# Performance work log

Hardware: AMD Instinct MI355X
Metric: run time of the kernel (lower is better)

Reference implementation:

```python
import jax, jax.numpy as jnp
import numpy as np

N = 50000      # nodes
E = 1600000    # edges (before self loops)
B = 512        # graphs
D = 128        # gcn dim (constant across the 3 GAT layers)
H = 1024       # hidden_dim
O = 128        # output_dim
NEG_SLOPE = 0.2


def setup_inputs() -> dict:
    key = jax.random.key(0)
    ks = jax.random.split(key, 24)
    inp = {
        "x": jax.random.normal(ks[0], (N, D), jnp.float32),
        "edge_index": jax.random.randint(ks[1], (2, E), 0, N, dtype=jnp.int64),
        "edge_weight": jax.random.uniform(ks[2], (E,), jnp.float32),
        "batch": jnp.sort(jax.random.randint(ks[3], (N,), 0, B, dtype=jnp.int64)),
    }
    s = 1.0 / np.sqrt(D)
    for i in range(3):
        k = 4 + 4 * i
        inp[f"W{i+1}"] = jax.random.normal(ks[k], (D, D), jnp.float32) * s
        inp[f"as{i+1}"] = jax.random.normal(ks[k + 1], (D,), jnp.float32) * s
        inp[f"ad{i+1}"] = jax.random.normal(ks[k + 2], (D,), jnp.float32) * s
        inp[f"b{i+1}"] = jnp.zeros((D,), jnp.float32)
    inp["Wf1"] = jax.random.normal(ks[16], (D, H), jnp.float32) * s
    inp["bf1"] = jnp.zeros((H,), jnp.float32)
    inp["Wf2"] = jax.random.normal(ks[17], (H, O), jnp.float32) * (1.0 / np.sqrt(H))
    inp["bf2"] = jnp.zeros((O,), jnp.float32)
    return inp


def gat_conv(x, src, dst, W, a_src, a_dst, b):
    """PyG GATConv, heads=1: gather -> leakyrelu -> segment softmax -> scatter-add."""
    h = x @ W                                   # [N, D]
    e = jax.nn.leaky_relu(jnp.take(h @ a_src, src) + jnp.take(h @ a_dst, dst), NEG_SLOPE)  # [E']
    m = jax.ops.segment_max(e, dst, num_segments=N)
    ex = jnp.exp(e - m[dst])
    denom = jax.ops.segment_sum(ex, dst, num_segments=N)
    alpha = ex / denom[dst]                      # segment softmax over incoming edges
    out = jax.ops.segment_sum(alpha[:, None] * h[src], dst, num_segments=N)
    return out + b


def reference(x, edge_index, edge_weight, batch,
              W1, as1, ad1, b1, W2, as2, ad2, b2, W3, as3, ad3, b3,
              Wf1, bf1, Wf2, bf2):
    # GATConv adds self loops; edge_weight is unused by GATConv (faithful to original)
    loop = jnp.arange(N, dtype=edge_index.dtype)
    src = jnp.concatenate([edge_index[0], loop])
    dst = jnp.concatenate([edge_index[1], loop])

    h = gat_conv(x, src, dst, W1, as1, ad1, b1)
    h = jax.nn.relu(gat_conv(h, src, dst, W2, as2, ad2, b2))
    h = jax.nn.relu(gat_conv(h, src, dst, W3, as3, ad3, b3))

    # global mean pool (gep)
    sums = jax.ops.segment_sum(h, batch, num_segments=B)        # [B, D]
    counts = jax.ops.segment_sum(jnp.ones((N,), h.dtype), batch, num_segments=B)
    pooled = sums / jnp.maximum(counts, 1.0)[:, None]

    # MLP head; dropout is identity at inference
    o = jax.nn.relu(pooled) @ Wf1 + bf1
    o = jax.nn.relu(o) @ Wf2 + bf2
    return o
```

## Files before the change

### kernel.cpp

```cpp
#include <hip/hip_runtime.h>
#include <cstdint>
#include <cstddef>

#define NEG_SLOPE 0.2f

typedef _Float16 f16x8 __attribute__((ext_vector_type(8)));
typedef float f32x4v __attribute__((ext_vector_type(4)));

__device__ __forceinline__ unsigned enc_f(float f) {
  unsigned u = __float_as_uint(f);
  return (u & 0x80000000u) ? ~u : (u | 0x80000000u);
}
__device__ __forceinline__ float dec_f(unsigned u) {
  return (u & 0x80000000u) ? __uint_as_float(u ^ 0x80000000u) : __uint_as_float(~u);
}

#define AST 136
#define WST 136
#define HST 132
#define SMEM_BYTES (64 * AST * 2 + 128 * WST * 2)

__global__ void k_bounds(const int* __restrict__ batch, int N, int B,
                         int* __restrict__ gstart, unsigned* __restrict__ maxPart,
                         int* __restrict__ counts) {
  int n = blockIdx.x * blockDim.x + threadIdx.x;
  if (n < 768) maxPart[n] = 0u;
  if (n >= N) return;
  counts[n] = 0;
  int cur = batch[n];
  if (n == 0) {
    for (int g = 0; g <= cur; g++) gstart[g] = 0;
  } else {
    int prev = batch[n - 1];
    for (int g = prev + 1; g <= cur; g++) gstart[g] = n;
  }
  if (n == N - 1) {
    for (int g = cur + 1; g <= B; g++) gstart[g] = N;
  }
}

__global__ void k_count_rank(const int* __restrict__ dst, int E,
                             int* counts, int* __restrict__ rank) {
  int e = blockIdx.x * blockDim.x + threadIdx.x;
  if (e < E) rank[e] = atomicAdd(&counts[dst[e]], 1);
}

__global__ __launch_bounds__(1024) void k_scan1(const int* __restrict__ counts, int N,
                                                int* __restrict__ row_ptr, int* __restrict__ part) {
  __shared__ int tmp[1024];
  int t = threadIdx.x;
  int i = blockIdx.x * 1024 + t;
  int v = (i < N) ? 1 + counts[i] : 0;
  tmp[t] = v;
  __syncthreads();
  for (int off = 1; off < 1024; off <<= 1) {
    int u = (t >= off) ? tmp[t - off] : 0;
    __syncthreads();
    tmp[t] += u;
    __syncthreads();
  }
  if (i < N) row_ptr[i + 1] = tmp[t];
  if (t == 1023) part[blockIdx.x] = tmp[t];
}

__global__ __launch_bounds__(1024) void k_scan3(int* __restrict__ row_ptr,
                                                const int* __restrict__ part, int N) {
  __shared__ int s_off;
  int bi = blockIdx.x;
  if (threadIdx.x == 0) {
    int run = 0;
    for (int b = 0; b < bi; b++) run += part[b];
    s_off = run;
    if (bi == 0) row_ptr[0] = 0;
  }
  __syncthreads();
  int i = bi * 1024 + threadIdx.x;
  if (i < N) row_ptr[i + 1] += s_off;
}

__device__ __forceinline__ void gemm_body(char* smem, float* redmax, int bx,
                                          const float* __restrict__ A32,
                                          const unsigned short* __restrict__ A16,
                                          const float* __restrict__ W,
                                          unsigned short* __restrict__ hb,
                                          const float* __restrict__ asrc,
                                          const float* __restrict__ adst,
                                          float* __restrict__ sv, float* __restrict__ dv,
                                          unsigned* __restrict__ maxSlot, int M) {
  _Float16* Ah = (_Float16*)smem;
  _Float16* Wt = (_Float16*)(smem + 64 * AST * 2);
  float*    hS = (float*)(smem + 64 * AST * 2);
  int t = threadIdx.x;
  int rowbase = bx * 64;

  if (A16) {
    for (int i = t; i < 64 * 16; i += 256) {
      int r = i >> 4, c8 = (i & 15) << 3;
      int gr = rowbase + r;
      uint4 v = make_uint4(0u, 0u, 0u, 0u);
      if (gr < M) v = *(const uint4*)&A16[(size_t)gr * 128 + c8];
      *(uint4*)&Ah[r * AST + c8] = v;
    }
  } else {
    for (int i = t; i < 64 * 32; i += 256) {
      int r = i >> 5, c4 = (i & 31) << 2;
      int gr = rowbase + r;
      float4 v = make_float4(0.f, 0.f, 0.f, 0.f);
      if (gr < M) v = *(const float4*)&A32[(size_t)gr * 128 + c4];
      _Float16 tmp[4] = {(_Float16)v.x, (_Float16)v.y, (_Float16)v.z, (_Float16)v.w};
      *(short4*)&Ah[r * AST + c4] = *(short4*)tmp;
    }
  }
  for (int i = t; i < 128 * 32; i += 256) {
    int r = i >> 5, c4 = (i & 31) << 2;
    float4 v = *(const float4*)&W[(size_t)r * 128 + c4];
    Wt[(c4 + 0) * WST + r] = (_Float16)v.x;
    Wt[(c4 + 1) * WST + r] = (_Float16)v.y;
    Wt[(c4 + 2) * WST + r] = (_Float16)v.z;
    Wt[(c4 + 3) * WST + r] = (_Float16)v.w;
  }
  __syncthreads();

  int wave = t >> 6, lane = t & 63, quad = lane >> 4, l15 = lane & 15;
  f32x4v acc[4][2];
#pragma unroll
  for (int mt = 0; mt < 4; mt++)
#pragma unroll
    for (int nt = 0; nt < 2; nt++) {
      acc[mt][nt][0] = 0.f; acc[mt][nt][1] = 0.f; acc[mt][nt][2] = 0.f; acc[mt][nt][3] = 0.f;
    }

#pragma unroll
  for (int s = 0; s < 4; s++) {
    int k0 = (s << 5) + (quad << 3);
    f16x8 af[4], bf[2];
#pragma unroll
    for (int mt = 0; mt < 4; mt++)
      af[mt] = *(f16x8*)&Ah[(mt * 16 + l15) * AST + k0];
#pragma unroll
    for (int nt = 0; nt < 2; nt++)
      bf[nt] = *(f16x8*)&Wt[(wave * 32 + nt * 16 + l15) * WST + k0];
#pragma unroll
    for (int mt = 0; mt < 4; mt++)
#pragma unroll
      for (int nt = 0; nt < 2; nt++)
        acc[mt][nt] = __builtin_amdgcn_mfma_f32_16x16x32_f16(af[mt], bf[nt], acc[mt][nt], 0, 0, 0);
  }
  __syncthreads();

#pragma unroll
  for (int mt = 0; mt < 4; mt++)
#pragma unroll
    for (int nt = 0; nt < 2; nt++)
#pragma unroll
      for (int rr = 0; rr < 4; rr++)
        hS[(mt * 16 + quad * 4 + rr) * HST + wave * 32 + nt * 16 + l15] = acc[mt][nt][rr];
  __syncthreads();

  int tx = t & 31, ty = t >> 5;
  float4 av  = *(const float4*)&asrc[tx * 4];
  float4 adv = *(const float4*)&adst[tx * 4];
  float wmax = -1e30f;
#pragma unroll
  for (int r8 = 0; r8 < 8; r8++) {
    int row = r8 * 8 + ty;
    int gr = rowbase + row;
    float4 hv = *(float4*)&hS[row * HST + tx * 4];
    float ps = hv.x * av.x + hv.y * av.y + hv.z * av.z + hv.w * av.w;
    float pd = hv.x * adv.x + hv.y * adv.y + hv.z * adv.z + hv.w * adv.w;
#pragma unroll
    for (int mask = 16; mask; mask >>= 1) {
      ps += __shfl_xor(ps, mask);
      pd += __shfl_xor(pd, mask);
    }
    if (gr < M) {
      _Float16 hq[4] = {(_Float16)hv.x, (_Float16)hv.y, (_Float16)hv.z, (_Float16)hv.w};
      *(uint2*)&hb[(size_t)gr * 128 + tx * 4] = *(uint2*)hq;
      if (tx == 0) { sv[gr] = ps; dv[gr] = pd; wmax = fmaxf(wmax, ps); }
    }
  }
#pragma unroll
  for (int mask = 32; mask; mask >>= 1) wmax = fmaxf(wmax, __shfl_xor(wmax, mask));
  if ((t & 63) == 0) redmax[t >> 6] = wmax;
  __syncthreads();
  if (t == 0) {
    float mx = fmaxf(fmaxf(redmax[0], redmax[1]), fmaxf(redmax[2], redmax[3]));
    atomicMax(&maxSlot[bx & 255], enc_f(mx));
  }
}

__global__ __launch_bounds__(256) void k_fill_gemm(const int* __restrict__ src,
                                                   const int* __restrict__ dst,
                                                   const int* __restrict__ rank, int E, int N,
                                                   const int* __restrict__ row_ptr,
                                                   int* __restrict__ col,
                                                   const float* __restrict__ A32,
                                                   const float* __restrict__ W,
                                                   unsigned short* __restrict__ hb,
                                                   const float* __restrict__ asrc,
                                                   const float* __restrict__ adst,
                                                   float* __restrict__ sv, float* __restrict__ dv,
                                                   unsigned* __restrict__ maxSlot, int Gg) {
  __shared__ __align__(16) char smem[SMEM_BYTES];
  __shared__ float redmax[4];
  int b = (int)blockIdx.x;
  bool isGemm = ((b % 9) == 4) && ((b / 9) < Gg);
  if (isGemm) {
    gemm_body(smem, redmax, b / 9, A32, (const unsigned short*)nullptr, W,
              hb, asrc, adst, sv, dv, maxSlot, N);
  } else {
    int nGemmBefore = (b >= 4) ? min((b - 4) / 9 + 1, Gg) : 0;
    int i = (b - nGemmBefore) * 256 + threadIdx.x;
    if (i < N) col[row_ptr[i]] = i;
    int e = i - N;
    if (e >= 0 && e < E) col[row_ptr[dst[e]] + 1 + rank[e]] = src[e];
  }
}

__global__ __launch_bounds__(256) void k_gemm_fused(const unsigned short* __restrict__ A16,
                                                    const float* __restrict__ W,
                                                    unsigned short* __restrict__ hb,
                                                    const float* __restrict__ asrc,
                                                    const float* __restrict__ adst,
                                                    float* __restrict__ sv, float* __restrict__ dv,
                                                    unsigned* __restrict__ maxSlot, int M) {
  __shared__ __align__(16) char smem[SMEM_BYTES];
  __shared__ float redmax[4];
  gemm_body(smem, redmax, (int)blockIdx.x, (const float*)nullptr, A16, W,
            hb, asrc, adst, sv, dv, maxSlot, M);
}

__global__ __launch_bounds__(256) void k_agg(const unsigned short* __restrict__ hb,
                                             const float* __restrict__ sv,
                                             const float* __restrict__ dv,
                                             const int* __restrict__ row_ptr,
                                             const int* __restrict__ col,
                                             const float* __restrict__ bias,
                                             const unsigned* __restrict__ maxSlot,
                                             unsigned short* __restrict__ out16,
                                             int N, int relu) {
  int wid = (int)((blockIdx.x * (size_t)blockDim.x + threadIdx.x) >> 6);
  int lane = threadIdx.x & 63;
  if (wid >= N) return;

  unsigned mp = max(max(maxSlot[lane], maxSlot[lane + 64]),
                    max(maxSlot[lane + 128], maxSlot[lane + 192]));
#pragma unroll
  for (int off = 32; off; off >>= 1) mp = max(mp, __shfl_xor(mp, off));
  float maxS = dec_f(mp);

  int beg = row_ptr[wid], end = row_ptr[wid + 1];
  float dn = dv[wid];
  float m = maxS + dn;
  m = (m > 0.f) ? m : NEG_SLOPE * m;

  int g = lane >> 4, sub = lane & 15;
  const uint32_t* hbu = (const uint32_t*)hb;
  float acc[8];
#pragma unroll
  for (int k = 0; k < 8; k++) acc[k] = 0.f;
  float dsum = 0.f;

  int j = beg + g;
  float w0 = 0.f, w1 = 0.f, w2 = 0.f;
  uint4 h0 = make_uint4(0u, 0u, 0u, 0u);
  uint4 h1 = make_uint4(0u, 0u, 0u, 0u);
  uint4 h2 = make_uint4(0u, 0u, 0u, 0u);
  if (j < end) {
    int sn = col[j];
    float e = sv[sn] + dn;
    e = (e > 0.f) ? e : NEG_SLOPE * e;
    w0 = __expf(e - m);
    h0 = *(const uint4*)(hbu + (size_t)sn * 64 + sub * 4);
  }
  if (j + 4 < end) {
    int sn = col[j + 4];
    float e = sv[sn] + dn;
    e = (e > 0.f) ? e : NEG_SLOPE * e;
    w1 = __expf(e - m);
    h1 = *(const uint4*)(hbu + (size_t)sn * 64 + sub * 4);
  }
  if (j + 8 < end) {
    int sn = col[j + 8];
    float e = sv[sn] + dn;
    e = (e > 0.f) ? e : NEG_SLOPE * e;
    w2 = __expf(e - m);
    h2 = *(const uint4*)(hbu + (size_t)sn * 64 + sub * 4);
  }
  j += 12;
  while (j < end) {
    dsum += w0;
    {
      const _Float16* hp = (const _Float16*)&h0;
#pragma unroll
      for (int k = 0; k < 8; k++) acc[k] += w0 * (float)hp[k];
    }
    w0 = w1; h0 = h1;
    w1 = w2; h1 = h2;
    int sn = col[j];
    float e = sv[sn] + dn;
    e = (e > 0.f) ? e : NEG_SLOPE * e;
    w2 = __expf(e - m);
    h2 = *(const uint4*)(hbu + (size_t)sn * 64 + sub * 4);
    j += 4;
  }
  {
    dsum += w0;
    const _Float16* hp = (const _Float16*)&h0;
#pragma unroll
    for (int k = 0; k < 8; k++) acc[k] += w0 * (float)hp[k];
  }
  {
    dsum += w1;
    const _Float16* hp = (const _Float16*)&h1;
#pragma unroll
    for (int k = 0; k < 8; k++) acc[k] += w1 * (float)hp[k];
  }
  {
    dsum += w2;
    const _Float16* hp = (const _Float16*)&h2;
#pragma unroll
    for (int k = 0; k < 8; k++) acc[k] += w2 * (float)hp[k];
  }

  dsum += __shfl_xor(dsum, 16);
  dsum += __shfl_xor(dsum, 32);
#pragma unroll
  for (int k = 0; k < 8; k++) {
    acc[k] += __shfl_xor(acc[k], 16);
    acc[k] += __shfl_xor(acc[k], 32);
  }
  if (lane < 16) {
    float inv = 1.f / dsum;
    float o[8];
    const float* bp = &bias[sub * 8];
#pragma unroll
    for (int k = 0; k < 8; k++) {
      o[k] = acc[k] * inv + bp[k];
      if (relu) o[k] = fmaxf(o[k], 0.f);
    }
    _Float16 q[8];
#pragma unroll
    for (int k = 0; k < 8; k++) q[k] = (_Float16)o[k];
    *(uint4*)&out16[(size_t)wid * 128 + sub * 8] = *(uint4*)q;
  }
}

__global__ __launch_bounds__(256) void k_pool(const unsigned short* __restrict__ h16,
                                              const int* __restrict__ gstart,
                                              float* __restrict__ pooled, int B) {
  __shared__ float red[4][128];
  int b = blockIdx.x, t = threadIdx.x;
  int c = t & 63, seg = t >> 6;
  int s0 = gstart[b], s1 = gstart[b + 1];
  int cnt = s1 - s0;
  int per = (cnt + 3) >> 2;
  int n0 = s0 + seg * per;
  int n1 = min(n0 + per, s1);
  const uint32_t* hu = (const uint32_t*)h16;
  float a0 = 0.f, a1 = 0.f;
  for (int n = n0; n < n1; n++) {
    union { uint32_t u; _Float16 h[2]; } cv;
    cv.u = hu[(size_t)n * 64 + c];
    a0 += (float)cv.h[0];
    a1 += (float)cv.h[1];
  }
  if (seg) { red[seg][2 * c] = a0; red[seg][2 * c + 1] = a1; }
  __syncthreads();
  if (seg == 0) {
    a0 += red[1][2 * c] + red[2][2 * c] + red[3][2 * c];
    a1 += red[1][2 * c + 1] + red[2][2 * c + 1] + red[3][2 * c + 1];
    float inv = 1.f / (float)(cnt > 0 ? cnt : 1);
    pooled[b * 128 + 2 * c]     = fmaxf(a0 * inv, 0.f);
    pooled[b * 128 + 2 * c + 1] = fmaxf(a1 * inv, 0.f);
  }
}

__global__ __launch_bounds__(256) void k_mlp(const float* __restrict__ pooled,
                                             const float* __restrict__ Wf1,
                                             const float* __restrict__ bf1,
                                             const float* __restrict__ Wf2,
                                             const float* __restrict__ bf2,
                                             float* __restrict__ out, int B) {
  __shared__ float P[4][128];
  __shared__ float H1[4][1024];
  __shared__ float R[4][128];
  int t = threadIdx.x;
  int g0 = blockIdx.x * 4;

  for (int i = t; i < 4 * 128; i += 256) {
    int gi = i >> 7, c = i & 127;
    P[gi][c] = (g0 + gi < B) ? pooled[(size_t)(g0 + gi) * 128 + c] : 0.f;
  }
  __syncthreads();

#pragma unroll
  for (int cb = 0; cb < 4; cb++) {
    int c = cb * 256 + t;
    float a0 = 0.f, a1 = 0.f, a2 = 0.f, a3 = 0.f;
    for (int k = 0; k < 128; k++) {
      float w = Wf1[(size_t)k * 1024 + c];
      a0 += P[0][k] * w; a1 += P[1][k] * w; a2 += P[2][k] * w; a3 += P[3][k] * w;
    }
    float b = bf1[c];
    H1[0][c] = fmaxf(a0 + b, 0.f);
    H1[1][c] = fmaxf(a1 + b, 0.f);
    H1[2][c] = fmaxf(a2 + b, 0.f);
    H1[3][c] = fmaxf(a3 + b, 0.f);
  }
  __syncthreads();

  int c = t & 127, hh = t >> 7;
  float a0 = 0.f, a1 = 0.f, a2 = 0.f, a3 = 0.f;
  int k0 = hh * 512;
  for (int k = k0; k < k0 + 512; k++) {
    float w = Wf2[(size_t)k * 128 + c];
    a0 += H1[0][k] * w; a1 += H1[1][k] * w; a2 += H1[2][k] * w; a3 += H1[3][k] * w;
  }
  if (hh == 1) { R[0][c] = a0; R[1][c] = a1; R[2][c] = a2; R[3][c] = a3; }
  __syncthreads();
  if (hh == 0) {
    float b = bf2[c];
    float o0 = a0 + R[0][c] + b;
    float o1 = a1 + R[1][c] + b;
    float o2 = a2 + R[2][c] + b;
    float o3 = a3 + R[3][c] + b;
    if (g0 + 0 < B) out[(size_t)(g0 + 0) * 128 + c] = o0;
    if (g0 + 1 < B) out[(size_t)(g0 + 1) * 128 + c] = o1;
    if (g0 + 2 < B) out[(size_t)(g0 + 2) * 128 + c] = o2;
    if (g0 + 3 < B) out[(size_t)(g0 + 3) * 128 + c] = o3;
  }
}

extern "C" void kernel_launch(void* const* d_in, const int* in_sizes, int n_in,
                              void* d_out, int out_size, void* d_ws, size_t ws_size,
                              hipStream_t stream) {
  const float* x     = (const float*)d_in[0];
  const int*   ei    = (const int*)d_in[1];
  const int*   batch = (const int*)d_in[3];
  const float* W1 = (const float*)d_in[4];
  const float* as1 = (const float*)d_in[5];
  const float* ad1 = (const float*)d_in[6];
  const float* b1 = (const float*)d_in[7];
  const float* W2 = (const float*)d_in[8];
  const float* as2 = (const float*)d_in[9];
  const float* ad2 = (const float*)d_in[10];
  const float* b2 = (const float*)d_in[11];
  const float* W3 = (const float*)d_in[12];
  const float* as3 = (const float*)d_in[13];
  const float* ad3 = (const float*)d_in[14];
  const float* b3 = (const float*)d_in[15];
  const float* Wf1 = (const float*)d_in[16];
  const float* bf1 = (const float*)d_in[17];
  const float* Wf2 = (const float*)d_in[18];
  const float* bf2 = (const float*)d_in[19];

  const int N = in_sizes[0] / 128;
  const int E = in_sizes[1] / 2;
  const int B = out_size / 128;

  char* base_ws = (char*)d_ws;
  size_t off = 0;
  auto carve = [&](size_t bytes) -> void* {
    off = (off + 255) & ~(size_t)255;
    void* p = base_ws + off;
    off += bytes;
    return p;
  };
  int* counts   = (int*)carve((size_t)N * 4);
  int* row_ptr  = (int*)carve((size_t)(N + 1) * 4);
  int* rank     = (int*)carve((size_t)E * 4);
  int* col      = (int*)carve((size_t)(E + N) * 4);
  int* part     = (int*)carve(1024 * 4);
  int* gstart   = (int*)carve((size_t)(B + 1) * 4);
  unsigned* maxPart = (unsigned*)carve(768 * 4);
  float* sbuf   = (float*)carve((size_t)N * 4);
  float* dbuf   = (float*)carve((size_t)N * 4);
  unsigned short* hb  = (unsigned short*)carve((size_t)N * 128 * 2);
  unsigned short* a16 = (unsigned short*)carve((size_t)N * 128 * 2);
  float* pooled = (float*)carve((size_t)B * 128 * 4);

  const int* srcp = ei;
  const int* dstp = ei + E;
  const int nb = (N + 1023) / 1024;
  const int Gg = (N + 63) / 64;
  const int Gf = (E + N + 255) / 256;

  hipLaunchKernelGGL(k_bounds, dim3((N + 255) / 256), dim3(256), 0, stream,
                     batch, N, B, gstart, maxPart, counts);
  hipLaunchKernelGGL(k_count_rank, dim3((E + 255) / 256), dim3(256), 0, stream,
                     dstp, E, counts, rank);
  hipLaunchKernelGGL(k_scan1, dim3(nb), dim3(1024), 0, stream, counts, N, row_ptr, part);
  hipLaunchKernelGGL(k_scan3, dim3(nb), dim3(1024), 0, stream, row_ptr, part, N);

  hipLaunchKernelGGL(k_fill_gemm, dim3(Gf + Gg), dim3(256), 0, stream,
                     srcp, dstp, rank, E, N, row_ptr, col,
                     x, W1, hb, as1, ad1, sbuf, dbuf, maxPart + 0 * 256, Gg);

  hipLaunchKernelGGL(k_agg, dim3((N + 3) / 4), dim3(256), 0, stream,
                     hb, sbuf, dbuf, row_ptr, col, b1, maxPart + 0 * 256, a16, N, 0);

  hipLaunchKernelGGL(k_gemm_fused, dim3(Gg), dim3(256), 0, stream,
                     a16, W2, hb, as2, ad2, sbuf, dbuf, maxPart + 1 * 256, N);
  hipLaunchKernelGGL(k_agg, dim3((N + 3) / 4), dim3(256), 0, stream,
                     hb, sbuf, dbuf, row_ptr, col, b2, maxPart + 1 * 256, a16, N, 1);

  hipLaunchKernelGGL(k_gemm_fused, dim3(Gg), dim3(256), 0, stream,
                     a16, W3, hb, as3, ad3, sbuf, dbuf, maxPart + 2 * 256, N);
  hipLaunchKernelGGL(k_agg, dim3((N + 3) / 4), dim3(256), 0, stream,
                     hb, sbuf, dbuf, row_ptr, col, b3, maxPart + 2 * 256, a16, N, 1);

  hipLaunchKernelGGL(k_pool, dim3(B), dim3(256), 0, stream, a16, gstart, pooled, B);
  hipLaunchKernelGGL(k_mlp, dim3((B + 3) / 4), dim3(256), 0, stream,
                     pooled, Wf1, bf1, Wf2, bf2, (float*)d_out, B);
}
```

Baseline: 527.9 us.

## Fuse preprocessing and pooling kernels to cut launch count

Zeroing of counts and maxPart moves to a single memset, and the edge count/rank pass is merged with the graph-bounds pass into one launch. The two-pass scan becomes a single kernel that recomputes each block's prefix offset by summing all earlier counts. Global mean pooling is folded into the MLP head kernel, which drops the pooled buffer. This removes several launches and intermediate round trips, but the scan now reads earlier counts redundantly in every block and the pool stage runs on only 128 blocks instead of 512.

```diff
diff --git a/kernel.cpp b/kernel.cpp
--- a/kernel.cpp
+++ b/kernel.cpp
@@ -20,36 +20,46 @@
 #define HST 132
 #define SMEM_BYTES (64 * AST * 2 + 128 * WST * 2)
 
-__global__ void k_bounds(const int* __restrict__ batch, int N, int B,
-                         int* __restrict__ gstart, unsigned* __restrict__ maxPart,
-                         int* __restrict__ counts) {
-  int n = blockIdx.x * blockDim.x + threadIdx.x;
-  if (n < 768) maxPart[n] = 0u;
-  if (n >= N) return;
-  counts[n] = 0;
-  int cur = batch[n];
-  if (n == 0) {
-    for (int g = 0; g <= cur; g++) gstart[g] = 0;
+__global__ void k_count_bounds(const int* __restrict__ dst, int E,
+                               int* counts, int* __restrict__ rank, int Ec,
+                               const int* __restrict__ batch, int N, int B,
+                               int* __restrict__ gstart) {
+  if ((int)blockIdx.x < Ec) {
+    int e = blockIdx.x * 256 + threadIdx.x;
+    if (e < E) rank[e] = atomicAdd(&counts[dst[e]], 1);
   } else {
-    int prev = batch[n - 1];
-    for (int g = prev + 1; g <= cur; g++) gstart[g] = n;
-  }
-  if (n == N - 1) {
-    for (int g = cur + 1; g <= B; g++) gstart[g] = N;
-  }
-}
-
-__global__ void k_count_rank(const int* __restrict__ dst, int E,
-                             int* counts, int* __restrict__ rank) {
-  int e = blockIdx.x * blockDim.x + threadIdx.x;
-  if (e < E) rank[e] = atomicAdd(&counts[dst[e]], 1);
-}
-
-__global__ __launch_bounds__(1024) void k_scan1(const int* __restrict__ counts, int N,
-                                                int* __restrict__ row_ptr, int* __restrict__ part) {
+    int n = (blockIdx.x - Ec) * 256 + threadIdx.x;
+    if (n >= N) return;
+    int cur = batch[n];
+    if (n == 0) {
+      for (int g = 0; g <= cur; g++) gstart[g] = 0;
+    } else {
+      int prev = batch[n - 1];
+      for (int g = prev + 1; g <= cur; g++) gstart[g] = n;
+    }
+    if (n == N - 1) {
+      for (int g = cur + 1; g <= B; g++) gstart[g] = N;
+    }
+  }
+}
+
+__global__ __launch_bounds__(1024) void k_scan_all(const int* __restrict__ counts, int N,
+                                                   int* __restrict__ row_ptr) {
   __shared__ int tmp[1024];
-  int t = threadIdx.x;
-  int i = blockIdx.x * 1024 + t;
+  __shared__ int s_off;
+  int bi = blockIdx.x, t = threadIdx.x;
+  int hi = bi * 1024;
+  int base = 0;
+  for (int i = t; i < hi; i += 1024) base += counts[i];
+  tmp[t] = base;
+  __syncthreads();
+  for (int off = 512; off; off >>= 1) {
+    if (t < off) tmp[t] += tmp[t + off];
+    __syncthreads();
+  }
+  if (t == 0) s_off = tmp[0] + hi;
+  __syncthreads();
+  int i = hi + t;
   int v = (i < N) ? 1 + counts[i] : 0;
   tmp[t] = v;
   __syncthreads();
@@ -59,23 +69,8 @@
     tmp[t] += u;
     __syncthreads();
   }
-  if (i < N) row_ptr[i + 1] = tmp[t];
-  if (t == 1023) part[blockIdx.x] = tmp[t];
-}
-
-__global__ __launch_bounds__(1024) void k_scan3(int* __restrict__ row_ptr,
-                                                const int* __restrict__ part, int N) {
-  __shared__ int s_off;
-  int bi = blockIdx.x;
-  if (threadIdx.x == 0) {
-    int run = 0;
-    for (int b = 0; b < bi; b++) run += part[b];
-    s_off = run;
-    if (bi == 0) row_ptr[0] = 0;
-  }
-  __syncthreads();
-  int i = bi * 1024 + threadIdx.x;
-  if (i < N) row_ptr[i + 1] += s_off;
+  if (i < N) row_ptr[i + 1] = tmp[t] + s_off;
+  if (bi == 0 && t == 0) row_ptr[0] = 0;
 }
 
 __device__ __forceinline__ void gemm_body(char* smem, float* redmax, int bx,
@@ -346,89 +341,85 @@
   }
 }
 
-__global__ __launch_bounds__(256) void k_pool(const unsigned short* __restrict__ h16,
-                                              const int* __restrict__ gstart,
-                                              float* __restrict__ pooled, int B) {
-  __shared__ float red[4][128];
-  int b = blockIdx.x, t = threadIdx.x;
-  int c = t & 63, seg = t >> 6;
-  int s0 = gstart[b], s1 = gstart[b + 1];
-  int cnt = s1 - s0;
-  int per = (cnt + 3) >> 2;
-  int n0 = s0 + seg * per;
-  int n1 = min(n0 + per, s1);
-  const uint32_t* hu = (const uint32_t*)h16;
-  float a0 = 0.f, a1 = 0.f;
-  for (int n = n0; n < n1; n++) {
-    union { uint32_t u; _Float16 h[2]; } cv;
-    cv.u = hu[(size_t)n * 64 + c];
-    a0 += (float)cv.h[0];
-    a1 += (float)cv.h[1];
-  }
-  if (seg) { red[seg][2 * c] = a0; red[seg][2 * c + 1] = a1; }
-  __syncthreads();
-  if (seg == 0) {
-    a0 += red[1][2 * c] + red[2][2 * c] + red[3][2 * c];
-    a1 += red[1][2 * c + 1] + red[2][2 * c + 1] + red[3][2 * c + 1];
-    float inv = 1.f / (float)(cnt > 0 ? cnt : 1);
-    pooled[b * 128 + 2 * c]     = fmaxf(a0 * inv, 0.f);
-    pooled[b * 128 + 2 * c + 1] = fmaxf(a1 * inv, 0.f);
-  }
-}
-
-__global__ __launch_bounds__(256) void k_mlp(const float* __restrict__ pooled,
-                                             const float* __restrict__ Wf1,
-                                             const float* __restrict__ bf1,
-                                             const float* __restrict__ Wf2,
-                                             const float* __restrict__ bf2,
-                                             float* __restrict__ out, int B) {
+__global__ __launch_bounds__(256) void k_poolmlp(const unsigned short* __restrict__ h16,
+                                                 const int* __restrict__ gstart,
+                                                 const float* __restrict__ Wf1,
+                                                 const float* __restrict__ bf1,
+                                                 const float* __restrict__ Wf2,
+                                                 const float* __restrict__ bf2,
+                                                 float* __restrict__ out, int B) {
   __shared__ float P[4][128];
   __shared__ float H1[4][1024];
   __shared__ float R[4][128];
+  __shared__ float red[4][128];
   int t = threadIdx.x;
   int g0 = blockIdx.x * 4;
-
-  for (int i = t; i < 4 * 128; i += 256) {
-    int gi = i >> 7, c = i & 127;
-    P[gi][c] = (g0 + gi < B) ? pooled[(size_t)(g0 + gi) * 128 + c] : 0.f;
-  }
-  __syncthreads();
+  int c = t & 63, seg = t >> 6;
+  const uint32_t* hu = (const uint32_t*)h16;
+
+  for (int gi = 0; gi < 4; gi++) {
+    int g = g0 + gi;
+    int s0 = 0, s1 = 0;
+    if (g < B) { s0 = gstart[g]; s1 = gstart[g + 1]; }
+    int cnt = s1 - s0;
+    int per = (cnt + 3) >> 2;
+    int n0 = s0 + seg * per;
+    int n1 = min(n0 + per, s1);
+    float a0 = 0.f, a1 = 0.f;
+    for (int n = n0; n < n1; n++) {
+      union { uint32_t u; _Float16 h[2]; } cv;
+      cv.u = hu[(size_t)n * 64 + c];
+      a0 += (float)cv.h[0];
+      a1 += (float)cv.h[1];
+    }
+    red[seg][2 * c] = a0;
+    red[seg][2 * c + 1] = a1;
+    __syncthreads();
+    if (seg == 0) {
+      float b0 = red[0][2 * c] + red[1][2 * c] + red[2][2 * c] + red[3][2 * c];
+      float b1 = red[0][2 * c + 1] + red[1][2 * c + 1] + red[2][2 * c + 1] + red[3][2 * c + 1];
+      float inv = 1.f / (float)(cnt > 0 ? cnt : 1);
+      P[gi][2 * c]     = fmaxf(b0 * inv, 0.f);
+      P[gi][2 * c + 1] = fmaxf(b1 * inv, 0.f);
+    }
+    __syncthreads();
+  }
 
 #pragma unroll
   for (int cb = 0; cb < 4; cb++) {
-    int c = cb * 256 + t;
+    int cc = cb * 256 + t;
     float a0 = 0.f, a1 = 0.f, a2 = 0.f, a3 = 0.f;
     for (int k = 0; k < 128; k++) {
-      float w = Wf1[(size_t)k * 1024 + c];
+      float w = Wf1[(size_t)k * 1024 + cc];
       a0 += P[0][k] * w; a1 += P[1][k] * w; a2 += P[2][k] * w; a3 += P[3][k] * w;
     }
-    float b = bf1[c];
-    H1[0][c] = fmaxf(a0 + b, 0.f);
-    H1[1][c] = fmaxf(a1 + b, 0.f);
-    H1[2][c] = fmaxf(a2 + b, 0.f);
-    H1[3][c] = fmaxf(a3 + b, 0.f);
-  }
-  __syncthreads();
-
-  int c = t & 127, hh = t >> 7;
+    float b = bf1[cc];
+    H1[0][cc] = fmaxf(a0 + b, 0.f);
+    H1[1][cc] = fmaxf(a1 + b, 0.f);
+    H1[2][cc] = fmaxf(a2 + b, 0.f);
+    H1[3][cc] = fmaxf(a3 + b, 0.f);
+  }
+  __syncthreads();
+
+  int cc = t & 127, hh = t >> 7;
   float a0 = 0.f, a1 = 0.f, a2 = 0.f, a3 = 0.f;
   int k0 = hh * 512;
   for (int k = k0; k < k0 + 512; k++) {
-    float w = Wf2[(size_t)k * 128 + c];
+    float w = Wf2[(size_t)k * 128 + cc];
     a0 += H1[0][k] * w; a1 += H1[1][k] * w; a2 += H1[2][k] * w; a3 += H1[3][k] * w;
   }
-  if (hh == 1) { R[0][c] = a0; R[1][c] = a1; R[2][c] = a2; R[3][c] = a3; }
+  if (hh == 1) { R[0][cc] = a0; R[1][cc] = a1; R[2][cc] = a2; R[3][cc] = a3; }
   __syncthreads();
   if (hh == 0) {
-    float b = bf2[c];
-    float o0 = a0 + R[0][c] + b;
-    float o1 = a1 + R[1][c] + b;
-    float o2 = a2 + R[2][c] + b;
-    float o3 = a3 + R[3][c] + b;
-    if (g0 + 0 < B) out[(size_t)(g0 + 0) * 128 + c] = o0;
-    if (g0 + 1 < B) out[(size_t)(g0 + 1) * 128 + c] = o1;
-    if (g0 + 2 < B) out[(size_t)(g0 + 2) * 128 + c] = o2;
-    if (g0 + 3 < B) out[(size_t)(g0 + 3) * 128 + c] = o3;
+    float b = bf2[cc];
+    float o0 = a0 + R[0][cc] + b;
+    float o1 = a1 + R[1][cc] + b;
+    float o2 = a2 + R[2][cc] + b;
+    float o3 = a3 + R[3][cc] + b;
+    if (g0 + 0 < B) out[(size_t)(g0 + 0) * 128 + cc] = o0;
+    if (g0 + 1 < B) out[(size_t)(g0 + 1) * 128 + cc] = o1;
+    if (g0 + 2 < B) out[(size_t)(g0 + 2) * 128 + cc] = o2;
+    if (g0 + 3 < B) out[(size_t)(g0 + 3) * 128 + cc] = o3;
   }
 }
 
@@ -468,30 +459,30 @@
     return p;
   };
   int* counts   = (int*)carve((size_t)N * 4);
+  unsigned* maxPart = (unsigned*)carve(768 * 4);
   int* row_ptr  = (int*)carve((size_t)(N + 1) * 4);
   int* rank     = (int*)carve((size_t)E * 4);
   int* col      = (int*)carve((size_t)(E + N) * 4);
-  int* part     = (int*)carve(1024 * 4);
   int* gstart   = (int*)carve((size_t)(B + 1) * 4);
-  unsigned* maxPart = (unsigned*)carve(768 * 4);
   float* sbuf   = (float*)carve((size_t)N * 4);
   float* dbuf   = (float*)carve((size_t)N * 4);
   unsigned short* hb  = (unsigned short*)carve((size_t)N * 128 * 2);
   unsigned short* a16 = (unsigned short*)carve((size_t)N * 128 * 2);
-  float* pooled = (float*)carve((size_t)B * 128 * 4);
 
   const int* srcp = ei;
   const int* dstp = ei + E;
   const int nb = (N + 1023) / 1024;
   const int Gg = (N + 63) / 64;
   const int Gf = (E + N + 255) / 256;
-
-  hipLaunchKernelGGL(k_bounds, dim3((N + 255) / 256), dim3(256), 0, stream,
-                     batch, N, B, gstart, maxPart, counts);
-  hipLaunchKernelGGL(k_count_rank, dim3((E + 255) / 256), dim3(256), 0, stream,
-                     dstp, E, counts, rank);
-  hipLaunchKernelGGL(k_scan1, dim3(nb), dim3(1024), 0, stream, counts, N, row_ptr, part);
-  hipLaunchKernelGGL(k_scan3, dim3(nb), dim3(1024), 0, stream, row_ptr, part, N);
+  const int Ec = (E + 255) / 256;
+  const int Nb = (N + 255) / 256;
+
+  size_t zspan = (size_t)((char*)(maxPart + 768) - (char*)counts);
+  hipMemsetAsync(counts, 0, zspan, stream);
+
+  hipLaunchKernelGGL(k_count_bounds, dim3(Ec + Nb), dim3(256), 0, stream,
+                     dstp, E, counts, rank, Ec, batch, N, B, gstart);
+  hipLaunchKernelGGL(k_scan_all, dim3(nb), dim3(1024), 0, stream, counts, N, row_ptr);
 
   hipLaunchKernelGGL(k_fill_gemm, dim3(Gf + Gg), dim3(256), 0, stream,
                      srcp, dstp, rank, E, N, row_ptr, col,
@@ -510,7 +501,6 @@
   hipLaunchKernelGGL(k_agg, dim3((N + 3) / 4), dim3(256), 0, stream,
                      hb, sbuf, dbuf, row_ptr, col, b3, maxPart + 2 * 256, a16, N, 1);
 
-  hipLaunchKernelGGL(k_pool, dim3(B), dim3(256), 0, stream, a16, gstart, pooled, B);
-  hipLaunchKernelGGL(k_mlp, dim3((B + 3) / 4), dim3(256), 0, stream,
-                     pooled, Wf1, bf1, Wf2, bf2, (float*)d_out, B);
-}
+  hipLaunchKernelGGL(k_poolmlp, dim3((B + 3) / 4), dim3(256), 0, stream,
+                     a16, gstart, Wf1, bf1, Wf2, bf2, (float*)d_out, B);
+}
```

Result: slower. 555.5 us (+5.2%).
